# Performance work log

Hardware: AMD Instinct MI355X
Metric: run time of the kernel (lower is better)

## Reference

```python
import jax, jax.numpy as jnp
import numpy as np

B, T, N, M, G = 4, 16, 256, 128, 8
D, H, FFN, FD = 512, 8, 1024, 256
HD = D // H
SCALE = HD ** -0.5
EPS = 1e-5
NL = 6  # num_layers; layer 0 has no self-attn


def _ln(x, g, b):
    mu = x.mean(-1, keepdims=True)
    var = ((x - mu) ** 2).mean(-1, keepdims=True)
    return (x - mu) * jax.lax.rsqrt(var + EPS) * g + b


def setup_inputs() -> dict:
    key = jax.random.key(0)
    ks = jax.random.split(key, 16)
    w = lambda i, shape: jax.random.normal(ks[i], shape, jnp.float32) * 0.02
    return {
        'current_tokens': jax.random.normal(ks[0], (B, T, N, D), jnp.float32),
        'trajectory_tokens': jax.random.normal(ks[1], (G, M, D), jnp.float32),
        'sa_in_w': w(2, (NL - 1, 3 * D, D)), 'sa_in_b': jnp.zeros((NL - 1, 3 * D), jnp.float32),
        'sa_out_w': w(3, (NL - 1, D, D)), 'sa_out_b': jnp.zeros((NL - 1, D), jnp.float32),
        'n1_g': jnp.ones((NL - 1, D), jnp.float32), 'n1_b': jnp.zeros((NL - 1, D), jnp.float32),
        'ca_qw': w(4, (NL, D, D)), 'ca_qb': jnp.zeros((NL, D), jnp.float32),
        'ca_kw': w(5, (NL, D, D)), 'ca_kb': jnp.zeros((NL, D), jnp.float32),
        'ca_vw': w(6, (NL, D, D)), 'ca_vb': jnp.zeros((NL, D), jnp.float32),
        'ca_ow': w(7, (NL, D, D)), 'ca_ob': jnp.zeros((NL, D), jnp.float32),
        'n2_g': jnp.ones((NL, D), jnp.float32), 'n2_b': jnp.zeros((NL, D), jnp.float32),
        'f_w1': w(8, (NL, FFN, D)), 'f_b1': jnp.zeros((NL, FFN), jnp.float32),
        'f_w2': w(9, (NL, D, FFN)), 'f_b2': jnp.zeros((NL, D), jnp.float32),
        'n3_g': jnp.ones((NL, D), jnp.float32), 'n3_b': jnp.zeros((NL, D), jnp.float32),
        'out_w': w(10, (FD, D)), 'out_b': jnp.zeros((FD,), jnp.float32),
        'on_g': jnp.ones((FD,), jnp.float32), 'on_b': jnp.zeros((FD,), jnp.float32),
    }


def reference(current_tokens, trajectory_tokens, sa_in_w, sa_in_b, sa_out_w, sa_out_b,
              n1_g, n1_b, ca_qw, ca_qb, ca_kw, ca_kb, ca_vw, ca_vb, ca_ow, ca_ob,
              n2_g, n2_b, f_w1, f_b1, f_w2, f_b2, n3_g, n3_b, out_w, out_b, on_g, on_b):
    x = current_tokens
    attn_list = []
    for i in range(NL):
        if i >= 1:  # self-attention over detections within each frame
            j = i - 1
            xf = x.reshape(B * T, N, D)
            qkv = xf @ sa_in_w[j].T + sa_in_b[j]
            q, k, v = jnp.split(qkv, 3, axis=-1)
            q = q.reshape(B * T, N, H, HD)
            k = k.reshape(B * T, N, H, HD)
            v = v.reshape(B * T, N, H, HD)
            s = jnp.einsum('bnhd,bmhd->bhnm', q, k) * SCALE
            a = jax.nn.softmax(s, axis=-1)
            o = jnp.einsum('bhnm,bmhd->bnhd', a, v).reshape(B * T, N, D)
            o = o @ sa_out_w[j].T + sa_out_b[j]
            x = _ln(x + o.reshape(B, T, N, D), n1_g[j], n1_b[j])
        # cross-attention against group-averaged trajectory memory
        Q = (x @ ca_qw[i].T + ca_qb[i]).reshape(B, T, N, H, HD)
        K = (trajectory_tokens @ ca_kw[i].T + ca_kb[i]).reshape(G, M, H, HD).mean(0)  # (M,H,HD)
        V = (trajectory_tokens @ ca_vw[i].T + ca_vb[i]).reshape(G, M, H, HD).mean(0)
        s = jnp.einsum('btnhd,mhd->btnhm', Q, K) * SCALE
        # current_times=None => rel_pe_mask is zeros(T,M): no future mask; rel_pe bias is dead code in source
        a = jax.nn.softmax(s, axis=-1)  # (B,T,N,H,M)
        o = jnp.einsum('btnhm,mhd->btnhd', a, V).reshape(B, T, N, D)
        o = o @ ca_ow[i].T + ca_ob[i]
        x = _ln(x + o, n2_g[i], n2_b[i])
        # FFN
        h = jax.nn.relu(x @ f_w1[i].T + f_b1[i]) @ f_w2[i].T + f_b2[i]
        x = _ln(x + h, n3_g[i], n3_b[i])
        attn_list.append(a.mean(axis=2))  # (B,T,H,M) avg over detections
    out = _ln(x @ out_w.T + out_b, on_g, on_b)
    return out, jnp.stack(attn_list)
```

## Files before the change

kernel.cpp:

```cpp
#include <hip/hip_runtime.h>
#include <cstdint>
#include <cstddef>

#define Bb 4
#define Tt 16
#define Nn 256
#define Mm 128
#define Gg 8
#define Dd 512
#define Hh 8
#define FFNf 1024
#define FDf 256
#define HDd 64
#define NLl 6
#define SCALEf 0.125f
#define EPSf 1e-5f

typedef __attribute__((ext_vector_type(8))) short short8;
typedef __attribute__((ext_vector_type(4))) float float4_;
typedef __attribute__((ext_vector_type(16))) float f32x16;
typedef __attribute__((ext_vector_type(4))) int int4_;
typedef __attribute__((ext_vector_type(2))) int int2_;

__device__ inline float b2f(ushort u){ union{uint i; float f;} v; v.i = ((uint)u)<<16; return v.f; }
__device__ inline ushort f2b(float f){ union{float f; uint i;} v; v.f=f; uint r = v.i + 0x7fffu + ((v.i>>16)&1u); return (ushort)(r>>16); }
__device__ inline void unpack2(uint w, float& lo, float& hi){
  union{uint i; float f;} a,b; a.i = w<<16; b.i = w & 0xffff0000u; lo=a.f; hi=b.f;
}
__device__ inline float wred(float v){
  #pragma unroll
  for(int m=32;m>=1;m>>=1) v += __shfl_xor(v, m, 64);
  return v;
}
__device__ inline f32x16 zero16(){
  f32x16 z;
  #pragma unroll
  for(int r=0;r<16;r++) z[r]=0.f;
  return z;
}
__device__ inline int xcd_swz(int orig, int nwg){
  int q = nwg >> 3, r = nwg & 7;
  int x = orig & 7, idx = orig >> 3;
  return (x < r ? x*(q+1) : r*(q+1) + (x-r)*q) + idx;
}

__global__ __launch_bounds__(256) void cvt_f2b(const float* __restrict__ in, ushort* __restrict__ out, int n){
  int i = (blockIdx.x*256 + threadIdx.x)*4;
  if (i+3 < n){
    float4_ v = *(const float4_*)(in+i);
    ushort o[4] = {f2b(v[0]),f2b(v[1]),f2b(v[2]),f2b(v[3])};
    *(int2_*)(out+i) = *(const int2_*)o;
  } else {
    for (; i<n; i++) out[i]=f2b(in[i]);
  }
}

__global__ __launch_bounds__(256) void tmean_k(const float* __restrict__ traj, ushort* __restrict__ tm){
  int idx = blockIdx.x*256 + threadIdx.x;
  float s = 0.f;
  #pragma unroll
  for(int g=0; g<8; g++) s += traj[g*65536 + idx];
  tm[idx] = f2b(s*0.125f);
}

template<int RELU>
__device__ __forceinline__ void gemm_core(
    const ushort* __restrict__ A, const ushort* __restrict__ W,
    const float* __restrict__ bias, ushort* __restrict__ C,
    int Ndim, int K, int rowA0, int colB0,
    ushort* As, ushort* Bs)
{
  const int tid = threadIdx.x;
  const int wid = tid>>6, lane = tid&63;
  const int wr = wid>>1, wc = wid&1;
  const int l15 = lane & 15, l4 = lane >> 4;

  const ushort* gA[2]; const ushort* gB[2];
  int ldsOff[2];
  #pragma unroll
  for (int s=0;s<2;s++){
    int p = wid*128 + s*64 + lane;
    int lrow = p>>3, x = p&7;
    int logical = x ^ (lrow&7);
    int row = (logical>>2)*64 + lrow;
    int ls = logical&3;
    gA[s] = A + (size_t)(rowA0+row)*K + ls*8;
    gB[s] = W + (size_t)(colB0+row)*K + ls*8;
    ldsOff[s] = wid*1024 + s*512;
  }

  float4_ acc[4][4];
  #pragma unroll
  for(int i=0;i<4;i++)
    #pragma unroll
    for(int j=0;j<4;j++){ acc[i][j][0]=0.f; acc[i][j][1]=0.f; acc[i][j][2]=0.f; acc[i][j][3]=0.f; }

  const int NT = K >> 5;
  #pragma unroll
  for (int s=0;s<2;s++){
    __builtin_amdgcn_global_load_lds((const unsigned int*)gA[s], (unsigned int*)(As + ldsOff[s]), 16, 0, 0);
    __builtin_amdgcn_global_load_lds((const unsigned int*)gB[s], (unsigned int*)(Bs + ldsOff[s]), 16, 0, 0);
    gA[s] += 32; gB[s] += 32;
  }
  __syncthreads();

  int cur = 0;
  for (int t=0; t<NT; ++t){
    if (t+1 < NT){
      #pragma unroll
      for (int s=0;s<2;s++){
        __builtin_amdgcn_global_load_lds((const unsigned int*)gA[s], (unsigned int*)(As + (cur^1)*4096 + ldsOff[s]), 16, 0, 0);
        __builtin_amdgcn_global_load_lds((const unsigned int*)gB[s], (unsigned int*)(Bs + (cur^1)*4096 + ldsOff[s]), 16, 0, 0);
        gA[s] += 32; gB[s] += 32;
      }
    }
    const ushort* Apt = As + cur*4096;
    const ushort* Bpt = Bs + cur*4096;
    short8 fa[4], fb[4];
    #pragma unroll
    for(int m=0;m<4;m++){
      int lrow = m*16 + l15;
      fa[m] = *(const short8*)&Apt[lrow*64 + (((wr*4 + l4) ^ (l15&7))*8)];
    }
    #pragma unroll
    for(int n=0;n<4;n++){
      int lrow = n*16 + l15;
      fb[n] = *(const short8*)&Bpt[lrow*64 + (((wc*4 + l4) ^ (l15&7))*8)];
    }
    #pragma unroll
    for(int m=0;m<4;m++)
      #pragma unroll
      for(int n=0;n<4;n++)
        acc[m][n] = __builtin_amdgcn_mfma_f32_16x16x32_bf16(fa[m], fb[n], acc[m][n], 0,0,0);
    if (t+1 < NT) __syncthreads();
    cur ^= 1;
  }

  #pragma unroll
  for(int m=0;m<4;m++){
    int grow = rowA0 + wr*64 + m*16 + l4*4;
    #pragma unroll
    for(int n=0;n<4;n++){
      int gcol = colB0 + wc*64 + n*16 + l15;
      float bv = bias[gcol];
      #pragma unroll
      for(int r=0;r<4;r++){
        float v = acc[m][n][r] + bv;
        if (RELU) v = fmaxf(v, 0.f);
        C[(size_t)(grow + r)*Ndim + gcol] = f2b(v);
      }
    }
  }
}

template<int RELU>
__global__ __launch_bounds__(256, 4) void gemm_bias(
    const ushort* __restrict__ A, const ushort* __restrict__ W,
    const float* __restrict__ bias, ushort* __restrict__ C,
    int Ndim, int K, int nbx)
{
  __shared__ ushort As[8192];
  __shared__ ushort Bs[8192];
  const int wg = xcd_swz(blockIdx.x, gridDim.x);
  const int bn = wg % nbx, bm = wg / nbx;
  gemm_core<RELU>(A, W, bias, C, Ndim, K, bm*128, bn*128, As, Bs);
}

__global__ __launch_bounds__(256, 4) void kv_all(
    const ushort* __restrict__ tm,
    const ushort* __restrict__ wk, const ushort* __restrict__ wv,
    const float* __restrict__ bk, const float* __restrict__ bv,
    ushort* __restrict__ KVm)
{
  __shared__ ushort As[8192];
  __shared__ ushort Bs[8192];
  const int i = blockIdx.x >> 3;
  const int r8 = blockIdx.x & 7;
  const int which = r8 >> 2, bn = r8 & 3;
  const ushort* W  = (which ? wv : wk) + (size_t)i*262144;
  const float* bias = (which ? bv : bk) + i*512;
  ushort* C = KVm + (size_t)(i*2 + which)*65536;
  gemm_core<0>(tm, W, bias, C, 512, 512, 0, bn*128, As, Bs);
}

template<int NKEYS, int WRITE_ATTN, int KPF>
__global__ __launch_bounds__(256) void attn_mfma(
  const ushort* __restrict__ Qb, int qstr,
  const ushort* __restrict__ Kb, int kstr,
  const ushort* __restrict__ Vb, int vstr,
  ushort* __restrict__ Ob,
  float* __restrict__ attn_out)
{
  constexpr int NK2 = NKEYS*2;
  __shared__ __align__(16) ushort KsV[NKEYS*64 + 64*NKEYS];
  __shared__ float psum[4][NKEYS];
  const int f = blockIdx.x, h = blockIdx.y;
  const int tid = threadIdx.x, lane = tid & 63, w = tid >> 6;
  const int l31 = lane & 31, l5 = lane >> 5;
  const int swz = (lane & 7) << 4;

  ushort* Ks = KsV;
  ushort* Vt = KsV + NKEYS*64;
  const ushort* kp0 = Kb + (size_t)(KPF ? f*256 : 0)*kstr + h*64;
  const ushort* vp0 = Vb + (size_t)(KPF ? f*256 : 0)*vstr + h*64;

  for (int c = tid; c < NKEYS*8; c += 256){
    int m = c>>3, dc = c&7;
    short8 k8 = *(const short8*)(kp0 + (size_t)m*kstr + dc*8);
    short8 v8 = *(const short8*)(vp0 + (size_t)m*vstr + dc*8);
    *(short8*)((char*)Ks + m*128 + ((dc*16) ^ ((m&7)<<4))) = k8;
    #pragma unroll
    for (int j=0;j<8;j++){
      int d = dc*8 + j;
      *(ushort*)((char*)Vt + d*NK2 + ((m*2) ^ (j<<4))) = (ushort)v8[j];
    }
  }

  short8 qb[2][4];
  const int q0 = w*64;
  const ushort* qp0 = Qb + (size_t)(f*256)*qstr + h*64;
  #pragma unroll
  for (int qj=0;qj<2;qj++)
    #pragma unroll
    for (int dc=0;dc<4;dc++)
      qb[qj][dc] = *(const short8*)(qp0 + (size_t)(q0 + qj*32 + l31)*qstr + dc*16 + l5*8);
  __syncthreads();

  f32x16 O[2][2];
  O[0][0]=zero16(); O[0][1]=zero16(); O[1][0]=zero16(); O[1][1]=zero16();
  float lpart[2] = {0.f, 0.f};

  for (int t = 0; t < NKEYS/32; t++){
    const int k0 = t*32;
    short8 ka[4];
    #pragma unroll
    for (int dc=0;dc<4;dc++)
      ka[dc] = *(const short8*)((char*)Ks + (k0+l31)*128 + (((dc*32) + (l5*16)) ^ swz));
    f32x16 s0 = zero16(), s1 = zero16();
    #pragma unroll
    for (int dc=0;dc<4;dc++){
      s0 = __builtin_amdgcn_mfma_f32_32x32x16_bf16(ka[dc], qb[0][dc], s0, 0,0,0);
      s1 = __builtin_amdgcn_mfma_f32_32x32x16_bf16(ka[dc], qb[1][dc], s1, 0,0,0);
    }
    uint pw[2][8];
    #pragma unroll
    for (int qj=0;qj<2;qj++){
      const f32x16& sv = qj ? s1 : s0;
      float p[16]; float lp = 0.f;
      #pragma unroll
      for (int r=0;r<16;r++){ p[r] = __expf(sv[r]*SCALEf); lp += p[r]; }
      lpart[qj] += lp;
      #pragma unroll
      for (int k=0;k<8;k++){
        uint w_;
        asm("v_cvt_pk_bf16_f32 %0, %1, %2" : "=v"(w_) : "v"(p[2*k]), "v"(p[2*k+1]));
        pw[qj][k] = w_;
      }
    }
    short8 pa[2][2];
    #pragma unroll
    for (int qj=0;qj<2;qj++){
      #pragma unroll
      for (int mj=0;mj<2;mj++){
        uint a0 = pw[qj][mj*4+2], b0 = pw[qj][mj*4+0];
        uint a1 = pw[qj][mj*4+3], b1 = pw[qj][mj*4+1];
        asm("v_permlane32_swap_b32 %0, %1" : "+v"(a0), "+v"(b0));
        asm("v_permlane32_swap_b32 %0, %1" : "+v"(a1), "+v"(b1));
        union { uint u[4]; short8 s8; } u_;
        u_.u[0]=b0; u_.u[1]=b1; u_.u[2]=a0; u_.u[3]=a1;
        pa[qj][mj] = u_.s8;
      }
    }
    #pragma unroll
    for (int mj=0;mj<2;mj++){
      short8 vbf[2];
      #pragma unroll
      for (int dj=0;dj<2;dj++)
        vbf[dj] = *(const short8*)((char*)Vt + (dj*32+l31)*NK2 + (((k0 + mj*16 + l5*8)*2) ^ swz));
      #pragma unroll
      for (int qj=0;qj<2;qj++)
        #pragma unroll
        for (int dj=0;dj<2;dj++)
          O[qj][dj] = __builtin_amdgcn_mfma_f32_32x32x16_bf16(pa[qj][mj], vbf[dj], O[qj][dj], 0,0,0);
    }
  }

  float invl[2];
  #pragma unroll
  for (int qj=0;qj<2;qj++){
    float lt = lpart[qj] + __shfl_xor(lpart[qj], 32, 64);
    invl[qj] = 1.f / lt;
  }

  ushort* op0 = Ob + (size_t)(f*256)*512 + h*64;
  #pragma unroll
  for (int qj=0;qj<2;qj++){
    #pragma unroll
    for (int r=0;r<16;r++){
      int qr = (r&3) + 8*(r>>2) + 4*l5;
      float il = __shfl(invl[qj], (lane & 32) | qr, 64);
      #pragma unroll
      for (int dj=0;dj<2;dj++){
        float v = O[qj][dj][r] * il;
        op0[(size_t)(q0 + qj*32 + qr)*512 + dj*32 + l31] = f2b(v);
      }
    }
  }

  if (WRITE_ATTN){
    for (int t = 0; t < NKEYS/32; t++){
      const int k0 = t*32;
      short8 ka[4];
      #pragma unroll
      for (int dc=0;dc<4;dc++)
        ka[dc] = *(const short8*)((char*)Ks + (k0+l31)*128 + (((dc*32) + (l5*16)) ^ swz));
      f32x16 s0 = zero16(), s1 = zero16();
      #pragma unroll
      for (int dc=0;dc<4;dc++){
        s0 = __builtin_amdgcn_mfma_f32_32x32x16_bf16(ka[dc], qb[0][dc], s0, 0,0,0);
        s1 = __builtin_amdgcn_mfma_f32_32x32x16_bf16(ka[dc], qb[1][dc], s1, 0,0,0);
      }
      float tsum[16];
      #pragma unroll
      for (int r=0;r<16;r++){
        float v = __expf(s0[r]*SCALEf)*invl[0] + __expf(s1[r]*SCALEf)*invl[1];
        #pragma unroll
        for (int mk=1; mk<=16; mk<<=1) v += __shfl_xor(v, mk, 64);
        tsum[r] = v;
      }
      if (l31 == 0){
        #pragma unroll
        for (int r=0;r<16;r++)
          psum[w][k0 + (r&3) + 8*(r>>2) + 4*l5] = tsum[r];
      }
    }
    __syncthreads();
    for (int m = tid; m < NKEYS; m += 256){
      attn_out[f*(Hh*NKEYS) + h*NKEYS + m] =
        (psum[0][m]+psum[1][m]+psum[2][m]+psum[3][m]) * (1.0f/256.0f);
    }
  }
}

__global__ __launch_bounds__(256) void ln_res(
  const ushort* __restrict__ X, const ushort* __restrict__ Oin,
  const float* __restrict__ g, const float* __restrict__ b,
  ushort* __restrict__ Y)
{
  const int row = blockIdx.x*4 + (threadIdx.x>>6);
  const int lane = threadIdx.x & 63;
  const ushort* xp = X + (size_t)row*512 + lane*8;
  const ushort* op = Oin + (size_t)row*512 + lane*8;
  uint xw[4], ow[4];
  *(int4_*)xw = *(const int4_*)xp;
  *(int4_*)ow = *(const int4_*)op;
  float v[8];
  #pragma unroll
  for(int j=0;j<4;j++){
    float xl,xh,ol,oh; unpack2(xw[j],xl,xh); unpack2(ow[j],ol,oh);
    v[2*j] = xl+ol; v[2*j+1] = xh+oh;
  }
  float s=0.f, sq=0.f;
  #pragma unroll
  for(int j=0;j<8;j++){ s += v[j]; sq += v[j]*v[j]; }
  s = wred(s); sq = wred(sq);
  float mu = s * (1.0f/512.0f);
  float var = sq * (1.0f/512.0f) - mu*mu;
  float rs = rsqrtf(var + EPSf);
  ushort ob[8];
  #pragma unroll
  for(int j=0;j<8;j++){
    float gg = g[lane*8+j], bb = b[lane*8+j];
    ob[j] = f2b((v[j]-mu)*rs*gg + bb);
  }
  *(int4_*)(Y + (size_t)row*512 + lane*8) = *(const int4_*)ob;
}

__global__ __launch_bounds__(256) void ln_out(
  const ushort* __restrict__ A, const float* __restrict__ g,
  const float* __restrict__ b, float* __restrict__ out)
{
  const int row = blockIdx.x*4 + (threadIdx.x>>6);
  const int lane = threadIdx.x & 63;
  uint aw[2];
  *(int2_*)aw = *(const int2_*)(A + (size_t)row*256 + lane*4);
  float v[4];
  unpack2(aw[0], v[0], v[1]); unpack2(aw[1], v[2], v[3]);
  float s=0.f, sq=0.f;
  #pragma unroll
  for(int j=0;j<4;j++){ s += v[j]; sq += v[j]*v[j]; }
  s = wred(s); sq = wred(sq);
  float mu = s * (1.0f/256.0f);
  float var = sq * (1.0f/256.0f) - mu*mu;
  float rs = rsqrtf(var + EPSf);
  float4_ o;
  #pragma unroll
  for(int j=0;j<4;j++){
    o[j] = (v[j]-mu)*rs*g[lane*4+j] + b[lane*4+j];
  }
  *(float4_*)(out + (size_t)row*256 + lane*4) = o;
}

static inline void cvt(const float* src, ushort* dst, int n, hipStream_t stream){
  cvt_f2b<<<(n/4 + 255)/256, 256, 0, stream>>>(src, dst, n);
}

extern "C" void kernel_launch(void* const* d_in, const int* in_sizes, int n_in,
                              void* d_out, int out_size, void* d_ws, size_t ws_size,
                              hipStream_t stream) {
  const float* cur      = (const float*)d_in[0];
  const float* traj     = (const float*)d_in[1];
  const float* sa_in_w  = (const float*)d_in[2];
  const float* sa_in_b  = (const float*)d_in[3];
  const float* sa_out_w = (const float*)d_in[4];
  const float* sa_out_b = (const float*)d_in[5];
  const float* n1_g     = (const float*)d_in[6];
  const float* n1_b     = (const float*)d_in[7];
  const float* ca_qw    = (const float*)d_in[8];
  const float* ca_qb    = (const float*)d_in[9];
  const float* ca_kw    = (const float*)d_in[10];
  const float* ca_kb    = (const float*)d_in[11];
  const float* ca_vw    = (const float*)d_in[12];
  const float* ca_vb    = (const float*)d_in[13];
  const float* ca_ow    = (const float*)d_in[14];
  const float* ca_ob    = (const float*)d_in[15];
  const float* n2_g     = (const float*)d_in[16];
  const float* n2_b     = (const float*)d_in[17];
  const float* f_w1     = (const float*)d_in[18];
  const float* f_b1     = (const float*)d_in[19];
  const float* f_w2     = (const float*)d_in[20];
  const float* f_b2     = (const float*)d_in[21];
  const float* n3_g     = (const float*)d_in[22];
  const float* n3_b     = (const float*)d_in[23];
  const float* out_w    = (const float*)d_in[24];
  const float* out_b    = (const float*)d_in[25];
  const float* on_g     = (const float*)d_in[26];
  const float* on_b     = (const float*)d_in[27];

  float* out      = (float*)d_out;
  float* attn_out = out + (size_t)Bb*Tt*Nn*FDf;

  uint8_t* ws = (uint8_t*)d_ws;
  size_t off = 0;
  auto alloc = [&](size_t bytes)->uint8_t*{ uint8_t* p = ws + off; off += (bytes + 255) & ~(size_t)255; return p; };
  ushort* X   = (ushort*)alloc(16777216);
  ushort* B1  = (ushort*)alloc(50331648);
  ushort* B2  = (ushort*)alloc(16777216);
  ushort* KVm = (ushort*)alloc((size_t)6*2*65536*2);
  ushort* tm  = (ushort*)alloc(131072);
  ushort* w_sa_in  = (ushort*)alloc((size_t)5*1536*512*2);
  ushort* w_sa_out = (ushort*)alloc((size_t)5*512*512*2);
  ushort* w_ca_q   = (ushort*)alloc((size_t)6*512*512*2);
  ushort* w_ca_k   = (ushort*)alloc((size_t)6*512*512*2);
  ushort* w_ca_v   = (ushort*)alloc((size_t)6*512*512*2);
  ushort* w_ca_o   = (ushort*)alloc((size_t)6*512*512*2);
  ushort* w_f1     = (ushort*)alloc((size_t)6*1024*512*2);
  ushort* w_f2     = (ushort*)alloc((size_t)6*512*1024*2);
  ushort* w_out    = (ushort*)alloc((size_t)256*512*2);

  cvt(cur,      X,        16384*512, stream);
  cvt(sa_in_w,  w_sa_in,  5*1536*512, stream);
  cvt(sa_out_w, w_sa_out, 5*512*512, stream);
  cvt(ca_qw,    w_ca_q,   6*512*512, stream);
  cvt(ca_kw,    w_ca_k,   6*512*512, stream);
  cvt(ca_vw,    w_ca_v,   6*512*512, stream);
  cvt(ca_ow,    w_ca_o,   6*512*512, stream);
  cvt(f_w1,     w_f1,     6*1024*512, stream);
  cvt(f_w2,     w_f2,     6*512*1024, stream);
  cvt(out_w,    w_out,    256*512, stream);
  tmean_k<<<256,256,0,stream>>>(traj, tm);
  kv_all<<<48,256,0,stream>>>(tm, w_ca_k, w_ca_v, ca_kb, ca_vb, KVm);

  for (int i=0;i<NLl;i++){
    if (i>=1){
      int j = i-1;
      gemm_bias<0><<<12*128,256,0,stream>>>(X, w_sa_in + (size_t)j*1536*512, sa_in_b + j*1536, B1, 1536, 512, 12);
      attn_mfma<256,0,1><<<dim3(64,8),256,0,stream>>>(B1, 1536, B1+512, 1536, B1+1024, 1536, B2, nullptr);
      gemm_bias<0><<<4*128,256,0,stream>>>(B2, w_sa_out + (size_t)j*262144, sa_out_b + j*512, B1, 512, 512, 4);
      ln_res<<<4096,256,0,stream>>>(X, B1, n1_g + j*512, n1_b + j*512, X);
    }
    gemm_bias<0><<<4*128,256,0,stream>>>(X, w_ca_q + (size_t)i*262144, ca_qb + i*512, B2, 512, 512, 4);
    attn_mfma<128,1,0><<<dim3(64,8),256,0,stream>>>(B2, 512, KVm + (size_t)i*131072, 512, KVm + (size_t)i*131072 + 65536, 512, B1, attn_out + (size_t)i*65536);
    gemm_bias<0><<<4*128,256,0,stream>>>(B1, w_ca_o + (size_t)i*262144, ca_ob + i*512, B2, 512, 512, 4);
    ln_res<<<4096,256,0,stream>>>(X, B2, n2_g + i*512, n2_b + i*512, X);
    gemm_bias<1><<<8*128,256,0,stream>>>(X, w_f1 + (size_t)i*524288, f_b1 + i*1024, B1, 1024, 512, 8);
    gemm_bias<0><<<4*128,256,0,stream>>>(B1, w_f2 + (size_t)i*524288, f_b2 + i*512, B2, 512, 1024, 4);
    ln_res<<<4096,256,0,stream>>>(X, B2, n3_g + i*512, n3_b + i*512, X);
  }
  gemm_bias<0><<<2*128,256,0,stream>>>(X, w_out, out_b, B2, 256, 512, 2);
  ln_out<<<4096,256,0,stream>>>(B2, on_g, on_b, out);
}
```

Before: 1.260 ms.

## Triple-buffer GEMM pipeline, fuse residual into epilogue, batch weight conversion

```diff
diff --git a/kernel.cpp b/kernel.cpp
--- a/kernel.cpp
+++ b/kernel.cpp
@@ -2,19 +2,10 @@
 #include <cstdint>
 #include <cstddef>
 
-#define Bb 4
-#define Tt 16
-#define Nn 256
-#define Mm 128
-#define Gg 8
-#define Dd 512
-#define Hh 8
-#define FFNf 1024
-#define FDf 256
-#define HDd 64
 #define NLl 6
 #define SCALEf 0.125f
 #define EPSf 1e-5f
+#define Hh 8
 
 typedef __attribute__((ext_vector_type(8))) short short8;
 typedef __attribute__((ext_vector_type(4))) float float4_;
@@ -44,15 +35,21 @@
   return (x < r ? x*(q+1) : r*(q+1) + (x-r)*q) + idx;
 }
 
-__global__ __launch_bounds__(256) void cvt_f2b(const float* __restrict__ in, ushort* __restrict__ out, int n){
-  int i = (blockIdx.x*256 + threadIdx.x)*4;
-  if (i+3 < n){
-    float4_ v = *(const float4_*)(in+i);
-    ushort o[4] = {f2b(v[0]),f2b(v[1]),f2b(v[2]),f2b(v[3])};
-    *(int2_*)(out+i) = *(const int2_*)o;
-  } else {
-    for (; i<n; i++) out[i]=f2b(in[i]);
-  }
+struct CvtTab {
+  const float* s[10];
+  ushort* d[10];
+  unsigned st[11];
+};
+__global__ __launch_bounds__(256) void cvt_all(CvtTab tab){
+  unsigned g = blockIdx.x*256 + threadIdx.x;
+  if (g >= tab.st[10]) return;
+  int i = 0;
+  #pragma unroll
+  for (int k=0;k<9;k++) if (g >= tab.st[k+1]) i = k+1;
+  unsigned off = g - tab.st[i];
+  float4_ v = *(const float4_*)(tab.s[i] + (size_t)off*4);
+  ushort o[4] = {f2b(v[0]),f2b(v[1]),f2b(v[2]),f2b(v[3])};
+  *(int2_*)(tab.d[i] + (size_t)off*4) = *(const int2_*)o;
 }
 
 __global__ __launch_bounds__(256) void tmean_k(const float* __restrict__ traj, ushort* __restrict__ tm){
@@ -63,10 +60,11 @@
   tm[idx] = f2b(s*0.125f);
 }
 
-template<int RELU>
+template<int RELU, int RESID>
 __device__ __forceinline__ void gemm_core(
     const ushort* __restrict__ A, const ushort* __restrict__ W,
-    const float* __restrict__ bias, ushort* __restrict__ C,
+    const float* __restrict__ bias, const ushort* __restrict__ R,
+    ushort* __restrict__ C,
     int Ndim, int K, int rowA0, int colB0,
     ushort* As, ushort* Bs)
 {
@@ -102,15 +100,26 @@
     __builtin_amdgcn_global_load_lds((const unsigned int*)gB[s], (unsigned int*)(Bs + ldsOff[s]), 16, 0, 0);
     gA[s] += 32; gB[s] += 32;
   }
-  __syncthreads();
+  if (NT > 1){
+    #pragma unroll
+    for (int s=0;s<2;s++){
+      __builtin_amdgcn_global_load_lds((const unsigned int*)gA[s], (unsigned int*)(As + 4096 + ldsOff[s]), 16, 0, 0);
+      __builtin_amdgcn_global_load_lds((const unsigned int*)gB[s], (unsigned int*)(Bs + 4096 + ldsOff[s]), 16, 0, 0);
+      gA[s] += 32; gB[s] += 32;
+    }
+  }
 
   int cur = 0;
   for (int t=0; t<NT; ++t){
-    if (t+1 < NT){
+    if (t+1 < NT) asm volatile("s_waitcnt vmcnt(4)" ::: "memory");
+    else          asm volatile("s_waitcnt vmcnt(0)" ::: "memory");
+    __builtin_amdgcn_s_barrier();
+    if (t+2 < NT){
+      int nb = cur+2; if (nb>=3) nb-=3;
       #pragma unroll
       for (int s=0;s<2;s++){
-        __builtin_amdgcn_global_load_lds((const unsigned int*)gA[s], (unsigned int*)(As + (cur^1)*4096 + ldsOff[s]), 16, 0, 0);
-        __builtin_amdgcn_global_load_lds((const unsigned int*)gB[s], (unsigned int*)(Bs + (cur^1)*4096 + ldsOff[s]), 16, 0, 0);
+        __builtin_amdgcn_global_load_lds((const unsigned int*)gA[s], (unsigned int*)(As + nb*4096 + ldsOff[s]), 16, 0, 0);
+        __builtin_amdgcn_global_load_lds((const unsigned int*)gB[s], (unsigned int*)(Bs + nb*4096 + ldsOff[s]), 16, 0, 0);
         gA[s] += 32; gB[s] += 32;
       }
     }
@@ -132,8 +141,7 @@
       #pragma unroll
       for(int n=0;n<4;n++)
         acc[m][n] = __builtin_amdgcn_mfma_f32_16x16x32_bf16(fa[m], fb[n], acc[m][n], 0,0,0);
-    if (t+1 < NT) __syncthreads();
-    cur ^= 1;
+    cur = (cur==2) ? 0 : cur+1;
   }
 
   #pragma unroll
@@ -146,6 +154,7 @@
       #pragma unroll
       for(int r=0;r<4;r++){
         float v = acc[m][n][r] + bv;
+        if (RESID) v += b2f(R[(size_t)(grow + r)*512 + gcol]);
         if (RELU) v = fmaxf(v, 0.f);
         C[(size_t)(grow + r)*Ndim + gcol] = f2b(v);
       }
@@ -153,34 +162,34 @@
   }
 }
 
-template<int RELU>
-__global__ __launch_bounds__(256, 4) void gemm_bias(
+template<int RELU, int RESID>
+__global__ __launch_bounds__(256, 3) void gemm_bias(
     const ushort* __restrict__ A, const ushort* __restrict__ W,
-    const float* __restrict__ bias, ushort* __restrict__ C,
-    int Ndim, int K, int nbx)
-{
-  __shared__ ushort As[8192];
-  __shared__ ushort Bs[8192];
+    const float* __restrict__ bias, const ushort* __restrict__ R,
+    ushort* __restrict__ C, int Ndim, int K, int nbx)
+{
+  __shared__ ushort As[12288];
+  __shared__ ushort Bs[12288];
   const int wg = xcd_swz(blockIdx.x, gridDim.x);
   const int bn = wg % nbx, bm = wg / nbx;
-  gemm_core<RELU>(A, W, bias, C, Ndim, K, bm*128, bn*128, As, Bs);
-}
-
-__global__ __launch_bounds__(256, 4) void kv_all(
+  gemm_core<RELU,RESID>(A, W, bias, R, C, Ndim, K, bm*128, bn*128, As, Bs);
+}
+
+__global__ __launch_bounds__(256, 3) void kv_all(
     const ushort* __restrict__ tm,
     const ushort* __restrict__ wk, const ushort* __restrict__ wv,
     const float* __restrict__ bk, const float* __restrict__ bv,
     ushort* __restrict__ KVm)
 {
-  __shared__ ushort As[8192];
-  __shared__ ushort Bs[8192];
+  __shared__ ushort As[12288];
+  __shared__ ushort Bs[12288];
   const int i = blockIdx.x >> 3;
   const int r8 = blockIdx.x & 7;
   const int which = r8 >> 2, bn = r8 & 3;
   const ushort* W  = (which ? wv : wk) + (size_t)i*262144;
   const float* bias = (which ? bv : bk) + i*512;
   ushort* C = KVm + (size_t)(i*2 + which)*65536;
-  gemm_core<0>(tm, W, bias, C, 512, 512, 0, bn*128, As, Bs);
+  gemm_core<0,0>(tm, W, bias, nullptr, C, 512, 512, 0, bn*128, As, Bs);
 }
 
 template<int NKEYS, int WRITE_ATTN, int KPF>
@@ -342,24 +351,18 @@
   }
 }
 
-__global__ __launch_bounds__(256) void ln_res(
-  const ushort* __restrict__ X, const ushort* __restrict__ Oin,
+__global__ __launch_bounds__(256) void ln_post(
+  const ushort* __restrict__ S,
   const float* __restrict__ g, const float* __restrict__ b,
   ushort* __restrict__ Y)
 {
   const int row = blockIdx.x*4 + (threadIdx.x>>6);
   const int lane = threadIdx.x & 63;
-  const ushort* xp = X + (size_t)row*512 + lane*8;
-  const ushort* op = Oin + (size_t)row*512 + lane*8;
-  uint xw[4], ow[4];
-  *(int4_*)xw = *(const int4_*)xp;
-  *(int4_*)ow = *(const int4_*)op;
+  uint xw[4];
+  *(int4_*)xw = *(const int4_*)(S + (size_t)row*512 + lane*8);
   float v[8];
   #pragma unroll
-  for(int j=0;j<4;j++){
-    float xl,xh,ol,oh; unpack2(xw[j],xl,xh); unpack2(ow[j],ol,oh);
-    v[2*j] = xl+ol; v[2*j+1] = xh+oh;
-  }
+  for(int j=0;j<4;j++){ unpack2(xw[j], v[2*j], v[2*j+1]); }
   float s=0.f, sq=0.f;
   #pragma unroll
   for(int j=0;j<8;j++){ s += v[j]; sq += v[j]*v[j]; }
@@ -370,8 +373,7 @@
   ushort ob[8];
   #pragma unroll
   for(int j=0;j<8;j++){
-    float gg = g[lane*8+j], bb = b[lane*8+j];
-    ob[j] = f2b((v[j]-mu)*rs*gg + bb);
+    ob[j] = f2b((v[j]-mu)*rs*g[lane*8+j] + b[lane*8+j]);
   }
   *(int4_*)(Y + (size_t)row*512 + lane*8) = *(const int4_*)ob;
 }
@@ -399,10 +401,6 @@
     o[j] = (v[j]-mu)*rs*g[lane*4+j] + b[lane*4+j];
   }
   *(float4_*)(out + (size_t)row*256 + lane*4) = o;
-}
-
-static inline void cvt(const float* src, ushort* dst, int n, hipStream_t stream){
-  cvt_f2b<<<(n/4 + 255)/256, 256, 0, stream>>>(src, dst, n);
 }
 
 extern "C" void kernel_launch(void* const* d_in, const int* in_sizes, int n_in,
@@ -438,7 +436,7 @@
   const float* on_b     = (const float*)d_in[27];
 
   float* out      = (float*)d_out;
-  float* attn_out = out + (size_t)Bb*Tt*Nn*FDf;
+  float* attn_out = out + (size_t)4*16*256*256;
 
   uint8_t* ws = (uint8_t*)d_ws;
   size_t off = 0;
@@ -458,35 +456,34 @@
   ushort* w_f2     = (ushort*)alloc((size_t)6*512*1024*2);
   ushort* w_out    = (ushort*)alloc((size_t)256*512*2);
 
-  cvt(cur,      X,        16384*512, stream);
-  cvt(sa_in_w,  w_sa_in,  5*1536*512, stream);
-  cvt(sa_out_w, w_sa_out, 5*512*512, stream);
-  cvt(ca_qw,    w_ca_q,   6*512*512, stream);
-  cvt(ca_kw,    w_ca_k,   6*512*512, stream);
-  cvt(ca_vw,    w_ca_v,   6*512*512, stream);
-  cvt(ca_ow,    w_ca_o,   6*512*512, stream);
-  cvt(f_w1,     w_f1,     6*1024*512, stream);
-  cvt(f_w2,     w_f2,     6*512*1024, stream);
-  cvt(out_w,    w_out,    256*512, stream);
+  CvtTab tab;
+  const float* srcs[10] = {cur, sa_in_w, sa_out_w, ca_qw, ca_kw, ca_vw, ca_ow, f_w1, f_w2, out_w};
+  ushort* dsts[10]      = {X,   w_sa_in, w_sa_out, w_ca_q, w_ca_k, w_ca_v, w_ca_o, w_f1, w_f2, w_out};
+  unsigned lens[10] = {16384u*512u, 5u*1536u*512u, 5u*512u*512u, 6u*512u*512u, 6u*512u*512u,
+                       6u*512u*512u, 6u*512u*512u, 6u*1024u*512u, 6u*512u*1024u, 256u*512u};
+  unsigned acc4 = 0;
+  for (int i=0;i<10;i++){ tab.s[i]=srcs[i]; tab.d[i]=dsts[i]; tab.st[i]=acc4; acc4 += lens[i]/4; }
+  tab.st[10] = acc4;
+  cvt_all<<<(acc4+255)/256,256,0,stream>>>(tab);
   tmean_k<<<256,256,0,stream>>>(traj, tm);
   kv_all<<<48,256,0,stream>>>(tm, w_ca_k, w_ca_v, ca_kb, ca_vb, KVm);
 
   for (int i=0;i<NLl;i++){
     if (i>=1){
       int j = i-1;
-      gemm_bias<0><<<12*128,256,0,stream>>>(X, w_sa_in + (size_t)j*1536*512, sa_in_b + j*1536, B1, 1536, 512, 12);
+      gemm_bias<0,0><<<12*128,256,0,stream>>>(X, w_sa_in + (size_t)j*1536*512, sa_in_b + j*1536, nullptr, B1, 1536, 512, 12);
       attn_mfma<256,0,1><<<dim3(64,8),256,0,stream>>>(B1, 1536, B1+512, 1536, B1+1024, 1536, B2, nullptr);
-      gemm_bias<0><<<4*128,256,0,stream>>>(B2, w_sa_out + (size_t)j*262144, sa_out_b + j*512, B1, 512, 512, 4);
-      ln_res<<<4096,256,0,stream>>>(X, B1, n1_g + j*512, n1_b + j*512, X);
-    }
-    gemm_bias<0><<<4*128,256,0,stream>>>(X, w_ca_q + (size_t)i*262144, ca_qb + i*512, B2, 512, 512, 4);
+      gemm_bias<0,1><<<4*128,256,0,stream>>>(B2, w_sa_out + (size_t)j*262144, sa_out_b + j*512, X, B1, 512, 512, 4);
+      ln_post<<<4096,256,0,stream>>>(B1, n1_g + j*512, n1_b + j*512, X);
+    }
+    gemm_bias<0,0><<<4*128,256,0,stream>>>(X, w_ca_q + (size_t)i*262144, ca_qb + i*512, nullptr, B2, 512, 512, 4);
     attn_mfma<128,1,0><<<dim3(64,8),256,0,stream>>>(B2, 512, KVm + (size_t)i*131072, 512, KVm + (size_t)i*131072 + 65536, 512, B1, attn_out + (size_t)i*65536);
-    gemm_bias<0><<<4*128,256,0,stream>>>(B1, w_ca_o + (size_t)i*262144, ca_ob + i*512, B2, 512, 512, 4);
-    ln_res<<<4096,256,0,stream>>>(X, B2, n2_g + i*512, n2_b + i*512, X);
-    gemm_bias<1><<<8*128,256,0,stream>>>(X, w_f1 + (size_t)i*524288, f_b1 + i*1024, B1, 1024, 512, 8);
-    gemm_bias<0><<<4*128,256,0,stream>>>(B1, w_f2 + (size_t)i*524288, f_b2 + i*512, B2, 512, 1024, 4);
-    ln_res<<<4096,256,0,stream>>>(X, B2, n3_g + i*512, n3_b + i*512, X);
-  }
-  gemm_bias<0><<<2*128,256,0,stream>>>(X, w_out, out_b, B2, 256, 512, 2);
+    gemm_bias<0,1><<<4*128,256,0,stream>>>(B1, w_ca_o + (size_t)i*262144, ca_ob + i*512, X, B2, 512, 512, 4);
+    ln_post<<<4096,256,0,stream>>>(B2, n2_g + i*512, n2_b + i*512, X);
+    gemm_bias<1,0><<<8*128,256,0,stream>>>(X, w_f1 + (size_t)i*524288, f_b1 + i*1024, nullptr, B1, 1024, 512, 8);
+    gemm_bias<0,1><<<4*128,256,0,stream>>>(B1, w_f2 + (size_t)i*524288, f_b2 + i*512, X, B2, 512, 1024, 4);
+    ln_post<<<4096,256,0,stream>>>(B2, n3_g + i*512, n3_b + i*512, X);
+  }
+  gemm_bias<0,0><<<2*128,256,0,stream>>>(X, w_out, out_b, nullptr, B2, 256, 512, 2);
   ln_out<<<4096,256,0,stream>>>(B2, on_g, on_b, out);
 }
```

Measured after the change: 1.316 ms. 4.5% more time.
